# Kernel tuning notes

Measured on AMD Instinct MI355X. Metric: run time of the kernel, lower is better.

Reference implementation:

```python
import jax, jax.numpy as jnp
from jax import lax
import numpy as np

B, NUM_TPM, NUM_CNV, NODE_DIM, DRUG_FEAT = 32, 16000, 16000, 36, 75
N_DRUGS, N_ATOMS, N_PAIRS = 128, 64, 4096


def setup_inputs() -> dict:
    key = jax.random.key(0)
    ks = jax.random.split(key, 32)

    def w(k, shape):
        fan_in = shape[0] if len(shape) == 2 else int(np.prod(shape[1:]))
        return (jax.random.normal(k, shape, jnp.float32) / np.float32(np.sqrt(fan_in))).astype(jnp.float32)

    pic_dim = jax.random.normal(ks[0], (B, 3, 256, 256), jnp.float32)
    rna_seq = jax.random.normal(ks[1], (B, NUM_TPM), jnp.float32)
    gene_cnv = jax.random.normal(ks[2], (B, NUM_CNV), jnp.float32)
    drug_fea = jax.random.uniform(ks[3], (N_DRUGS, N_ATOMS, DRUG_FEAT), jnp.float32)
    a = (jax.random.uniform(ks[4], (N_DRUGS, N_ATOMS, N_ATOMS)) < 0.15).astype(jnp.float32)
    drug_adj = jnp.maximum(a, jnp.transpose(a, (0, 2, 1)))
    index_list = jnp.stack([
        jax.random.randint(ks[5], (N_PAIRS,), 0, B),
        jax.random.randint(ks[6], (N_PAIRS,), 0, N_DRUGS)], axis=1)
    target = jax.random.randint(ks[7], (N_PAIRS,), 0, 2)
    logit_scale = jnp.asarray(10.0, jnp.float32)
    return dict(
        pic_dim=pic_dim, rna_seq=rna_seq, gene_cnv=gene_cnv,
        drug_fea=drug_fea, drug_adj=drug_adj, index_list=index_list,
        target=target, logit_scale=logit_scale,
        conv_w=w(ks[8], (32, 3, 5, 5)), conv_b=jnp.zeros((32,), jnp.float32),
        fc1_w=w(ks[9], (32 * 128 * 128, 1024)), fc1_b=jnp.zeros((1024,), jnp.float32),
        fc2_w=w(ks[10], (1024, 36)), fc2_b=jnp.zeros((36,), jnp.float32),
        mlp1_w1=w(ks[11], (NUM_TPM, NUM_TPM // 4)), mlp1_b1=jnp.zeros((NUM_TPM // 4,), jnp.float32),
        mlp1_w2=w(ks[12], (NUM_TPM // 4, NODE_DIM)), mlp1_b2=jnp.zeros((NODE_DIM,), jnp.float32),
        mlp2_w1=w(ks[13], (NUM_CNV, NUM_CNV // 4)), mlp2_b1=jnp.zeros((NUM_CNV // 4,), jnp.float32),
        mlp2_w2=w(ks[14], (NUM_CNV // 4, NODE_DIM)), mlp2_b2=jnp.zeros((NODE_DIM,), jnp.float32),
        att_w1=w(ks[15], (36, 128)), att_b1=jnp.zeros((128,), jnp.float32),
        att_w2=w(ks[16], (128, 1)),
        end_w1=w(ks[17], (NODE_DIM * 4, NODE_DIM)), end_b1=jnp.zeros((NODE_DIM,), jnp.float32),
        end_w2=w(ks[18], (NODE_DIM, 2)), end_b2=jnp.zeros((2,), jnp.float32),
        gcn_w=w(ks[19], (DRUG_FEAT, NODE_DIM * 8)), gcn_w2=w(ks[20], (NODE_DIM * 8, NODE_DIM * 2)))


def _mlp(x, w1, b1, w2, b2):  # Linear-ReLU-(Dropout eval)-Linear-Softmax
    h = jax.nn.relu(x @ w1 + b1)
    return jax.nn.softmax(h @ w2 + b2, axis=-1)


def _ce(logits, labels):  # mean cross entropy, labels int [N]
    lp = jax.nn.log_softmax(logits, axis=-1)
    return -jnp.take_along_axis(lp, labels[:, None], axis=1).mean()


def reference(pic_dim, rna_seq, gene_cnv, drug_fea, drug_adj, index_list, target,
              logit_scale, conv_w, conv_b, fc1_w, fc1_b, fc2_w, fc2_b,
              mlp1_w1, mlp1_b1, mlp1_w2, mlp1_b2, mlp2_w1, mlp2_b1, mlp2_w2, mlp2_b2,
              att_w1, att_b1, att_w2, end_w1, end_b1, end_w2, end_b2, gcn_w, gcn_w2):
    # omics branches
    rna1 = _mlp(rna_seq, mlp1_w1, mlp1_b1, mlp1_w2, mlp1_b2)    # [B,36]
    cnv1 = _mlp(gene_cnv, mlp2_w1, mlp2_b1, mlp2_w2, mlp2_b2)   # [B,36]
    # image branch: conv(3->32,k5,p2) + relu + maxpool2 + fc
    x = lax.conv_general_dilated(pic_dim, conv_w, (1, 1), [(2, 2), (2, 2)])
    x = jax.nn.relu(x + conv_b[None, :, None, None])
    x = lax.reduce_window(x, -jnp.inf, lax.max, (1, 1, 2, 2), (1, 1, 2, 2), 'VALID')
    x = x.reshape(x.shape[0], -1)                               # [B, 32*128*128]
    x = jax.nn.relu(x @ fc1_w + fc1_b)
    pic1 = x @ fc2_w + fc2_b                                    # [B,36]
    # semantic attention over the two omics views
    z = jnp.stack([rna1, cnv1], axis=1)                         # [B,2,36]
    wv = (jnp.tanh(z @ att_w1 + att_b1) @ att_w2).mean(0)       # [2,1]
    beta = jax.nn.softmax(wv, axis=0)
    cell = (beta[None] * z).sum(1)                              # [B,36]
    # CLIP-style loss
    pic1 = pic1 / jnp.linalg.norm(pic1, axis=1, keepdims=True)
    cell = cell / jnp.linalg.norm(cell, axis=1, keepdims=True)
    image_fea = logit_scale * (pic1 @ cell.T)
    labels = jnp.arange(image_fea.shape[0])
    total_loss2 = (_ce(image_fea, labels) + _ce(image_fea.T, labels)) / 2
    cell_cat = jnp.concatenate([cell, pic1], axis=1)            # [B,72]
    # batched drug GCN (replaces per-drug python loop)
    eye = jnp.eye(N_ATOMS, dtype=jnp.float32)
    def gcn_one(X, A):
        Ht = A.T * (1.0 - eye) + eye        # set diagonal to 1 (add self loops)
        deg = Ht.sum(1)
        dinv = jnp.where(deg == 0, 0.0, 1.0 / deg)
        Hn = dinv[:, None] * Ht             # D^-1 A_hat  (== H.t() after norm)
        out = Hn @ ((Hn @ (X @ gcn_w)) @ gcn_w2)
        return jnp.max(jax.nn.relu(out), axis=0)  # max over atoms -> [72]
    drugfea = jax.vmap(gcn_one)(drug_fea, drug_adj)             # [n_drugs,72]
    # pair prediction head
    Bc = jnp.concatenate([cell_cat[index_list[:, 0]], drugfea[index_list[:, 1]]], axis=1)
    Bp = _mlp(Bc, end_w1, end_b1, end_w2, end_b2)               # [n_pairs,2]
    loss1 = _ce(Bp, target)
    return (loss1, total_loss2, Bp, target)
```

## Files before the change

### kernel.cpp

```cpp
#include <hip/hip_runtime.h>
#include <hip/hip_bf16.h>
#include <math.h>

typedef float evf4 __attribute__((ext_vector_type(4)));
typedef float evf2 __attribute__((ext_vector_type(2)));

__device__ __forceinline__ void fma4(float4& a, float s, const float4& v) {
  a.x += s * v.x; a.y += s * v.y; a.z += s * v.z; a.w += s * v.w;
}
__device__ __forceinline__ float4 ntload4(const float4* p) {
  evf4 v = __builtin_nontemporal_load((const evf4*)p);
  return make_float4(v.x, v.y, v.z, v.w);
}
__device__ __forceinline__ float2 ntload2(const float2* p) {
  evf2 v = __builtin_nontemporal_load((const evf2*)p);
  return make_float2(v.x, v.y);
}

__device__ __forceinline__ void conv_body(
    const float* __restrict__ pic, const float* __restrict__ cw,
    const float* __restrict__ cb, float* __restrict__ pooled,
    int bid, float tile[3][8][260]) {
  int php = bid & 63, ocg2 = (bid >> 6) & 1, b = bid >> 7;
  int tid = threadIdx.x;
  int pw = tid & 127, phl = tid >> 7;
  int ph = php * 2 + phl;
  int h_base = php * 4 - 2;
  for (int i = tid; i < 3 * 8 * 260; i += 256) {
    int c = i % 260; int rr = (i / 260) & 7; int ic = i / (260 * 8);
    int h = h_base + rr, w = c - 2;
    float v = 0.f;
    if (h >= 0 && h < 256 && w >= 0 && w < 256)
      v = pic[((size_t)b * 3 + ic) * 65536 + h * 256 + w];
    tile[ic][rr][c] = v;
  }
  __syncthreads();
  float acc[16][4];
#pragma unroll
  for (int o = 0; o < 16; ++o)
#pragma unroll
    for (int q = 0; q < 4; ++q) acc[o][q] = 0.f;
  int r0 = phl * 2;
  int c0 = pw * 2;
#pragma unroll
  for (int ic = 0; ic < 3; ++ic) {
    float win[6][6];
#pragma unroll
    for (int r = 0; r < 6; ++r)
#pragma unroll
      for (int cc = 0; cc < 6; ++cc) win[r][cc] = tile[ic][r0 + r][c0 + cc];
#pragma unroll
    for (int o = 0; o < 16; ++o) {
      const float* __restrict__ wk = cw + ((ocg2 * 16 + o) * 3 + ic) * 25;
#pragma unroll
      for (int kh = 0; kh < 5; ++kh)
#pragma unroll
        for (int kw = 0; kw < 5; ++kw) {
          float wv = wk[kh * 5 + kw];
          acc[o][0] += win[kh][kw] * wv;
          acc[o][1] += win[kh][kw + 1] * wv;
          acc[o][2] += win[kh + 1][kw] * wv;
          acc[o][3] += win[kh + 1][kw + 1] * wv;
        }
    }
  }
#pragma unroll
  for (int o = 0; o < 16; ++o) {
    float m = fmaxf(fmaxf(acc[o][0], acc[o][1]), fmaxf(acc[o][2], acc[o][3]));
    m = fmaxf(m + cb[ocg2 * 16 + o], 0.f);
    pooled[(((size_t)b * 32 + ocg2 * 16 + o) * 128 + ph) * 128 + pw] = m;
  }
}

__device__ __forceinline__ void wc_body(
    const float* __restrict__ w1, const float* __restrict__ w2,
    float* __restrict__ wc, int bx) {
  int i = bx * 256 + threadIdx.x;
  if (i >= 75 * 72) return;
  int r = i / 72, c = i - r * 72;
  float s = 0.f;
  for (int k = 0; k < 288; ++k) s += w1[r * 288 + k] * w2[k * 72 + c];
  wc[i] = s;
}

__global__ __launch_bounds__(256) void k1_conv_wc_kernel(
    const float* __restrict__ pic, const float* __restrict__ cw,
    const float* __restrict__ cb, float* __restrict__ pooled,
    const float* __restrict__ gw, const float* __restrict__ gw2,
    float* __restrict__ wcb) {
  __shared__ float tile[3][8][260];
  int bid = blockIdx.x;
  if (bid < 4096) conv_body(pic, cw, cb, pooled, bid, tile);
  else            wc_body(gw, gw2, wcb, bid - 4096);
}

__device__ __forceinline__ void gemm2c_body(
    const float* __restrict__ X, const float* __restrict__ W,
    float* __restrict__ partial, int K, int N, int chunk,
    int bx, int split, float xs[128][36]) {
  int tid = threadIdx.x;
  int colv = bx * 256 + tid;
  int col0 = colv * 2;
  bool active = col0 < N;
  int k0 = split * chunk, k1 = min(k0 + chunk, K);
  size_t Nv = (size_t)(N >> 1);
  const float2* Wv = (const float2*)W;
  float2 acc[32];
#pragma unroll
  for (int b = 0; b < 32; ++b) acc[b] = make_float2(0.f, 0.f);

  auto fmablk = [&](int kk, const float2& w2) {
    const float4* xr = (const float4*)xs[kk];
#pragma unroll
    for (int b4 = 0; b4 < 8; ++b4) {
      float4 xv = xr[b4];
      acc[b4 * 4 + 0].x += xv.x * w2.x; acc[b4 * 4 + 0].y += xv.x * w2.y;
      acc[b4 * 4 + 1].x += xv.y * w2.x; acc[b4 * 4 + 1].y += xv.y * w2.y;
      acc[b4 * 4 + 2].x += xv.z * w2.x; acc[b4 * 4 + 2].y += xv.z * w2.y;
      acc[b4 * 4 + 3].x += xv.w * w2.x; acc[b4 * 4 + 3].y += xv.w * w2.y;
    }
  };

  for (int kt = k0; kt < k1; kt += 128) {
    __syncthreads();
#pragma unroll
    for (int j = 0; j < 4; ++j) {
      int idx = tid + j * 256;
      int b = idx >> 5, kk = (idx & 31) * 4;
      float4 x = *(const float4*)&X[(size_t)b * K + kt + kk];
      xs[kk + 0][b] = x.x; xs[kk + 1][b] = x.y;
      xs[kk + 2][b] = x.z; xs[kk + 3][b] = x.w;
    }
    __syncthreads();
    if (active) {
      const float2* wp = Wv + (size_t)kt * Nv + colv;
      float2 cur[8], nxt[8];
#pragma unroll
      for (int j = 0; j < 8; ++j) cur[j] = ntload2(wp + (size_t)j * Nv);
#pragma unroll 1
      for (int g = 0; g < 15; ++g) {
        const float2* wn = wp + 8 * Nv;
#pragma unroll
        for (int j = 0; j < 8; ++j) nxt[j] = ntload2(wn + (size_t)j * Nv);
        int kb = g * 8;
#pragma unroll
        for (int j = 0; j < 8; ++j) fmablk(kb + j, cur[j]);
#pragma unroll
        for (int j = 0; j < 8; ++j) cur[j] = nxt[j];
        wp = wn;
      }
#pragma unroll
      for (int j = 0; j < 8; ++j) fmablk(120 + j, cur[j]);
    }
  }
  if (active) {
    float* p = partial + (size_t)split * 32 * N + col0;
#pragma unroll
    for (int b = 0; b < 32; ++b) *(float2*)(p + (size_t)b * N) = acc[b];
  }
}

__global__ __launch_bounds__(256) void gemm_all_kernel(
    const float* __restrict__ pooled, const float* __restrict__ fc1w,
    float* __restrict__ pfc1,
    const float* __restrict__ rna, const float* __restrict__ m1w1, float* __restrict__ pm1,
    const float* __restrict__ cnv, const float* __restrict__ m2w1, float* __restrict__ pm2) {
  __shared__ float xs[128][36];
  int b = blockIdx.x;
  if (b < 512) {
    gemm2c_body(pooled, fc1w, pfc1, 524288, 1024, 2048, b & 1, b >> 1, xs);
  } else {
    int j = b - 512;
    int z = j / 504;
    int r = j % 504;
    int bx = r & 7, split = r >> 3;
    if (z == 0) gemm2c_body(rna, m1w1, pm1, 16000, 4000, 256, bx, split, xs);
    else        gemm2c_body(cnv, m2w1, pm2, 16000, 4000, 256, bx, split, xs);
  }
}

__device__ __forceinline__ void fadd4(float4& a, const float4& v) {
  a.x += v.x; a.y += v.y; a.z += v.z; a.w += v.w;
}

__device__ __forceinline__ void reduce_s1_body(
    const float* __restrict__ partial, float* __restrict__ p2,
    int bx, int sy) {
  int i = bx * 256 + threadIdx.x;
  const float4* p = (const float4*)partial + (size_t)(sy * 128) * 8192 + i;
  const size_t st = 8192;
  float4 s0 = make_float4(0, 0, 0, 0), s1 = s0, s2 = s0, s3 = s0;
  for (int sp = 0; sp < 128; sp += 4) {
    fadd4(s0, ntload4(p + (sp + 0) * st));
    fadd4(s1, ntload4(p + (sp + 1) * st));
    fadd4(s2, ntload4(p + (sp + 2) * st));
    fadd4(s3, ntload4(p + (sp + 3) * st));
  }
  float4 r;
  r.x = (s0.x + s1.x) + (s2.x + s3.x);
  r.y = (s0.y + s1.y) + (s2.y + s3.y);
  r.z = (s0.z + s1.z) + (s2.z + s3.z);
  r.w = (s0.w + s1.w) + (s2.w + s3.w);
  ((float4*)p2)[(size_t)sy * 8192 + i] = r;
}

__device__ __forceinline__ void reduce_mlp_body(
    const float* __restrict__ partial, const float* __restrict__ bias,
    float* __restrict__ out, int bx) {
  int i = bx * 256 + threadIdx.x;
  if (i >= 32000) return;
  const float4* p = (const float4*)partial + i;
  const size_t st = 32000;
  float4 s0 = make_float4(0, 0, 0, 0), s1 = s0, s2 = s0, s3 = s0;
  int sp = 0;
  for (; sp + 4 <= 63; sp += 4) {
    fadd4(s0, ntload4(p + (sp + 0) * st));
    fadd4(s1, ntload4(p + (sp + 1) * st));
    fadd4(s2, ntload4(p + (sp + 2) * st));
    fadd4(s3, ntload4(p + (sp + 3) * st));
  }
  for (; sp < 63; ++sp) fadd4(s0, ntload4(p + (size_t)sp * st));
  float4 bi = ((const float4*)bias)[i % 1000];
  float4 r;
  r.x = fmaxf(bi.x + (s0.x + s1.x) + (s2.x + s3.x), 0.f);
  r.y = fmaxf(bi.y + (s0.y + s1.y) + (s2.y + s3.y), 0.f);
  r.z = fmaxf(bi.z + (s0.z + s1.z) + (s2.z + s3.z), 0.f);
  r.w = fmaxf(bi.w + (s0.w + s1.w) + (s2.w + s3.w), 0.f);
  ((float4*)out)[i] = r;
}

__global__ __launch_bounds__(256) void k3_reduce_kernel(
    const float* __restrict__ pfc1, float* __restrict__ p2fc1,
    const float* __restrict__ pm1, const float* __restrict__ m1b1, float* __restrict__ h1,
    const float* __restrict__ pm2, const float* __restrict__ m2b1, float* __restrict__ h2) {
  int b = blockIdx.x;
  if (b < 64) {
    reduce_s1_body(pfc1, p2fc1, b & 31, b >> 5);
  } else {
    int idx = b - 64;
    if (idx < 125) reduce_mlp_body(pm1, m1b1, h1, idx);
    else           reduce_mlp_body(pm2, m2b1, h2, idx - 125);
  }
}

__device__ __forceinline__ void reduce_s2_body(
    const float* __restrict__ p2, const float* __restrict__ bias,
    float* __restrict__ out, int bx) {
  int i = bx * 256 + threadIdx.x;
  float4 a = ((const float4*)p2)[i];
  float4 b = ((const float4*)p2)[8192 + i];
  float4 bi = ((const float4*)bias)[i & 255];
  float4 r;
  r.x = fmaxf(bi.x + a.x + b.x, 0.f);
  r.y = fmaxf(bi.y + a.y + b.y, 0.f);
  r.z = fmaxf(bi.z + a.z + b.z, 0.f);
  r.w = fmaxf(bi.w + a.w + b.w, 0.f);
  ((float4*)out)[i] = r;
}

__device__ __forceinline__ void gcn_body(
    const float* __restrict__ Xg, const float* __restrict__ Ag,
    const float* __restrict__ Wc, float* __restrict__ drugfea, int d,
    float Hn[64][65], float Xs[64][75], float Wcs[75][72],
    float Ys[64][72], float Ts[64][72]) {
  int tid = threadIdx.x;
  const float* Ad = Ag + (size_t)d * 4096;
  const float* Xd = Xg + (size_t)d * 4800;
  for (int i = tid; i < 4096; i += 256) {
    int r = i & 63, c = i >> 6;
    Hn[r][c] = (r == c) ? 1.f : Ad[c * 64 + r];
  }
  for (int i = tid; i < 4800; i += 256) Xs[i / 75][i % 75] = Xd[i];
  for (int i = tid; i < 5400; i += 256) Wcs[i / 72][i % 72] = Wc[i];
  __syncthreads();
  if (tid < 64) {
    float s = 0.f;
    for (int c = 0; c < 64; ++c) s += Hn[tid][c];
    float inv = (s == 0.f) ? 0.f : 1.f / s;
    for (int c = 0; c < 64; ++c) Hn[tid][c] *= inv;
  }
  __syncthreads();
  int rb = tid >> 3, cb = tid & 7;
  int r0 = rb * 2, c0 = cb * 9;
  {
    float o0[9], o1[9];
#pragma unroll
    for (int j = 0; j < 9; ++j) { o0[j] = 0.f; o1[j] = 0.f; }
    for (int k = 0; k < 75; ++k) {
      float x0 = Xs[r0][k], x1 = Xs[r0 + 1][k];
#pragma unroll
      for (int j = 0; j < 9; ++j) {
        float w = Wcs[k][c0 + j];
        o0[j] += x0 * w; o1[j] += x1 * w;
      }
    }
#pragma unroll
    for (int j = 0; j < 9; ++j) { Ys[r0][c0 + j] = o0[j]; Ys[r0 + 1][c0 + j] = o1[j]; }
  }
  __syncthreads();
  {
    float o0[9], o1[9];
#pragma unroll
    for (int j = 0; j < 9; ++j) { o0[j] = 0.f; o1[j] = 0.f; }
    for (int k = 0; k < 64; ++k) {
      float x0 = Hn[r0][k], x1 = Hn[r0 + 1][k];
#pragma unroll
      for (int j = 0; j < 9; ++j) {
        float w = Ys[k][c0 + j];
        o0[j] += x0 * w; o1[j] += x1 * w;
      }
    }
#pragma unroll
    for (int j = 0; j < 9; ++j) { Ts[r0][c0 + j] = o0[j]; Ts[r0 + 1][c0 + j] = o1[j]; }
  }
  __syncthreads();
  {
    float o0[9], o1[9];
#pragma unroll
    for (int j = 0; j < 9; ++j) { o0[j] = 0.f; o1[j] = 0.f; }
    for (int k = 0; k < 64; ++k) {
      float x0 = Hn[r0][k], x1 = Hn[r0 + 1][k];
#pragma unroll
      for (int j = 0; j < 9; ++j) {
        float w = Ts[k][c0 + j];
        o0[j] += x0 * w; o1[j] += x1 * w;
      }
    }
#pragma unroll
    for (int j = 0; j < 9; ++j) {
      Ys[r0][c0 + j] = fmaxf(o0[j], 0.f);
      Ys[r0 + 1][c0 + j] = fmaxf(o1[j], 0.f);
    }
  }
  __syncthreads();
  if (tid < 72) {
    float m = Ys[0][tid];
    for (int i = 1; i < 64; ++i) m = fmaxf(m, Ys[i][tid]);
    drugfea[d * 72 + tid] = m;
  }
}

__global__ __launch_bounds__(256) void k4_s2_gcn_kernel(
    const float* __restrict__ p2fc1, const float* __restrict__ fc1_b,
    float* __restrict__ fcact,
    const float* __restrict__ Xg, const float* __restrict__ Ag,
    const float* __restrict__ wcb, float* __restrict__ drugfea) {
  __shared__ float Hn[64][65];
  __shared__ float Xs[64][75];
  __shared__ float Wcs[75][72];
  __shared__ float Ys[64][72];
  __shared__ float Ts[64][72];
  int b = blockIdx.x;
  if (b < 32) reduce_s2_body(p2fc1, fc1_b, fcact, b);
  else        gcn_body(Xg, Ag, wcb, drugfea, b - 32, Hn, Xs, Wcs, Ys, Ts);
}

__global__ __launch_bounds__(256) void lin36_all_kernel(
    const float* __restrict__ X0, const float* __restrict__ W0,
    const float* __restrict__ bi0, float* __restrict__ out0,
    const float* __restrict__ X1, const float* __restrict__ W1,
    const float* __restrict__ bi1, float* __restrict__ out1,
    const float* __restrict__ X2, const float* __restrict__ W2,
    const float* __restrict__ bi2, float* __restrict__ out2) {
  const float* X; const float* W; const float* bias; float* out; int K; bool do_sm;
  if (blockIdx.y == 0)      { X = X0; W = W0; bias = bi0; out = out0; K = 4000; do_sm = true; }
  else if (blockIdx.y == 1) { X = X1; W = W1; bias = bi1; out = out1; K = 4000; do_sm = true; }
  else                      { X = X2; W = W2; bias = bi2; out = out2; K = 1024; do_sm = false; }
  __shared__ float xs[4000];
  __shared__ float red[28][36];
  __shared__ float vals[36];
  __shared__ float mxv, smv;
  int b = blockIdx.x, tid = threadIdx.x;
  for (int i = tid; i < K; i += 256) xs[i] = X[(size_t)b * K + i];
  __syncthreads();
  if (tid < 252) {
    int c4 = tid % 9, g = tid / 9;
    const float4* W4 = (const float4*)W;
    float4 s = make_float4(0.f, 0.f, 0.f, 0.f);
    for (int k = g; k < K; k += 28) fma4(s, xs[k], W4[k * 9 + c4]);
    red[g][c4 * 4 + 0] = s.x; red[g][c4 * 4 + 1] = s.y;
    red[g][c4 * 4 + 2] = s.z; red[g][c4 * 4 + 3] = s.w;
  }
  __syncthreads();
  if (tid < 36) {
    float s = bias[tid];
    for (int g = 0; g < 28; ++g) s += red[g][tid];
    vals[tid] = s;
  }
  __syncthreads();
  if (do_sm) {
    if (tid == 0) {
      float m = -1e30f;
      for (int j = 0; j < 36; ++j) m = fmaxf(m, vals[j]);
      float e = 0.f;
      for (int j = 0; j < 36; ++j) e += expf(vals[j] - m);
      mxv = m; smv = e;
    }
    __syncthreads();
    if (tid < 36) out[b * 36 + tid] = expf(vals[tid] - mxv) / smv;
  } else {
    if (tid < 36) out[b * 36 + tid] = vals[tid];
  }
}

__global__ __launch_bounds__(256) void head_kernel(
    const float* __restrict__ rna1, const float* __restrict__ cnv1,
    const float* __restrict__ pic1r, const float* __restrict__ aw1,
    const float* __restrict__ ab1, const float* __restrict__ aw2,
    const float* __restrict__ scale_p, float* __restrict__ cell_cat,
    float* __restrict__ dout) {
  __shared__ float z[2][32][36];
  __shared__ float pic1n[32][36];
  __shared__ float celln[32][36];
  __shared__ float fea[32][32];
  __shared__ float wvp[64];
  __shared__ float beta0, beta1;
  __shared__ float rowl[32], coll[32];
  int tid = threadIdx.x;
  for (int i = tid; i < 1152; i += 256) {
    int b = i / 36, k = i - (i / 36) * 36;
    z[0][b][k] = rna1[i];
    z[1][b][k] = cnv1[i];
    pic1n[b][k] = pic1r[i];
  }
  __syncthreads();
  {
    int p = tid >> 2, sub = tid & 3;
    int b = p >> 1, v = p & 1;
    float s = 0.f;
    for (int h = sub; h < 128; h += 4) {
      float a = ab1[h];
      for (int k = 0; k < 36; ++k) a += z[v][b][k] * aw1[k * 128 + h];
      s += tanhf(a) * aw2[h];
    }
    s += __shfl_down(s, 1, 64);
    s += __shfl_down(s, 2, 64);
    if (sub == 0) wvp[p] = s;
  }
  __syncthreads();
  if (tid == 0) {
    float w0 = 0.f, w1 = 0.f;
    for (int b = 0; b < 32; ++b) { w0 += wvp[b * 2]; w1 += wvp[b * 2 + 1]; }
    w0 /= 32.f; w1 /= 32.f;
    float m = fmaxf(w0, w1);
    float e0 = expf(w0 - m), e1 = expf(w1 - m);
    beta0 = e0 / (e0 + e1); beta1 = e1 / (e0 + e1);
  }
  __syncthreads();
  for (int i = tid; i < 1152; i += 256) {
    int b = i / 36, k = i - (i / 36) * 36;
    celln[b][k] = beta0 * z[0][b][k] + beta1 * z[1][b][k];
  }
  __syncthreads();
  if (tid < 32) {
    float s = 0.f;
    for (int k = 0; k < 36; ++k) { float x = pic1n[tid][k]; s += x * x; }
    float inv = 1.f / sqrtf(s);
    for (int k = 0; k < 36; ++k) pic1n[tid][k] *= inv;
  } else if (tid < 64) {
    int b = tid - 32;
    float s = 0.f;
    for (int k = 0; k < 36; ++k) { float x = celln[b][k]; s += x * x; }
    float inv = 1.f / sqrtf(s);
    for (int k = 0; k < 36; ++k) celln[b][k] *= inv;
  }
  __syncthreads();
  for (int i = tid; i < 1152; i += 256) {
    int b = i / 36, k = i - (i / 36) * 36;
    cell_cat[b * 72 + k] = celln[b][k];
    cell_cat[b * 72 + 36 + k] = pic1n[b][k];
  }
  float sc = *scale_p;
  for (int t = tid; t < 1024; t += 256) {
    int i = t >> 5, j = t & 31;
    float s = 0.f;
    for (int k = 0; k < 36; ++k) s += pic1n[i][k] * celln[j][k];
    fea[i][j] = sc * s;
  }
  __syncthreads();
  if (tid < 32) {
    float m = -1e30f;
    for (int j = 0; j < 32; ++j) m = fmaxf(m, fea[tid][j]);
    float e = 0.f;
    for (int j = 0; j < 32; ++j) e += expf(fea[tid][j] - m);
    rowl[tid] = (logf(e) + m) - fea[tid][tid];
  } else if (tid < 64) {
    int j = tid - 32;
    float m = -1e30f;
    for (int i = 0; i < 32; ++i) m = fmaxf(m, fea[i][j]);
    float e = 0.f;
    for (int i = 0; i < 32; ++i) e += expf(fea[i][j] - m);
    coll[j] = (logf(e) + m) - fea[j][j];
  }
  __syncthreads();
  if (tid == 0) {
    float s1 = 0.f, s2 = 0.f;
    for (int i = 0; i < 32; ++i) { s1 += rowl[i]; s2 += coll[i]; }
    dout[1] = 0.5f * (s1 / 32.f + s2 / 32.f);
  }
}

__global__ __launch_bounds__(256) void pair_kernel(
    const float* __restrict__ cell_cat, const float* __restrict__ drugfea,
    const int* __restrict__ idx, const int* __restrict__ target,
    const float* __restrict__ w1, const float* __restrict__ b1,
    const float* __restrict__ w2, const float* __restrict__ b2,
    float* __restrict__ bp_out, float* __restrict__ tgt_out,
    float* __restrict__ blocksums) {
  __shared__ float w1s[144][36];
  __shared__ float ccs[32][73];
  __shared__ float dfs[128][73];
  __shared__ float w2s[72], b2s[2];
  __shared__ float lsum[256];
  int tid = threadIdx.x;
  {
    float4* dst = (float4*)&w1s[0][0];
    const float4* src = (const float4*)w1;
    for (int i = tid; i < 1296; i += 256) dst[i] = src[i];
  }
  for (int i = tid; i < 2304; i += 256) ccs[i / 72][i % 72] = cell_cat[i];
  for (int i = tid; i < 9216; i += 256) dfs[i / 72][i % 72] = drugfea[i];
  if (tid < 72) w2s[tid] = w2[tid];
  if (tid < 2) b2s[tid] = b2[tid];
  __syncthreads();
  int p = blockIdx.x * 256 + tid;
  int ci = idx[p * 2], dj = idx[p * 2 + 1];
  float4 h4[9];
  {
    const float4* bb = (const float4*)b1;
#pragma unroll
    for (int q = 0; q < 9; ++q) h4[q] = bb[q];
  }
  for (int k = 0; k < 72; ++k) {
    float x = ccs[ci][k];
    const float4* wr = (const float4*)&w1s[k][0];
#pragma unroll
    for (int q = 0; q < 9; ++q) fma4(h4[q], x, wr[q]);
  }
  for (int k = 0; k < 72; ++k) {
    float x = dfs[dj][k];
    const float4* wr = (const float4*)&w1s[72 + k][0];
#pragma unroll
    for (int q = 0; q < 9; ++q) fma4(h4[q], x, wr[q]);
  }
  float l0 = b2s[0], l1 = b2s[1];
#pragma unroll
  for (int q = 0; q < 9; ++q) {
    float hv;
    hv = fmaxf(h4[q].x, 0.f); l0 += hv * w2s[(q * 4 + 0) * 2]; l1 += hv * w2s[(q * 4 + 0) * 2 + 1];
    hv = fmaxf(h4[q].y, 0.f); l0 += hv * w2s[(q * 4 + 1) * 2]; l1 += hv * w2s[(q * 4 + 1) * 2 + 1];
    hv = fmaxf(h4[q].z, 0.f); l0 += hv * w2s[(q * 4 + 2) * 2]; l1 += hv * w2s[(q * 4 + 2) * 2 + 1];
    hv = fmaxf(h4[q].w, 0.f); l0 += hv * w2s[(q * 4 + 3) * 2]; l1 += hv * w2s[(q * 4 + 3) * 2 + 1];
  }
  float m = fmaxf(l0, l1);
  float e0 = expf(l0 - m), e1 = expf(l1 - m);
  float inv = 1.f / (e0 + e1);
  float p0 = e0 * inv, p1 = e1 * inv;
  bp_out[p * 2] = p0;
  bp_out[p * 2 + 1] = p1;
  int t = target[p];
  float mm = fmaxf(p0, p1);
  float lse = logf(expf(p0 - mm) + expf(p1 - mm)) + mm;
  float chosen = t ? p1 : p0;
  lsum[tid] = lse - chosen;
  tgt_out[p] = (float)t;
  __syncthreads();
  for (int s = 128; s > 0; s >>= 1) {
    if (tid < s) lsum[tid] += lsum[tid + s];
    __syncthreads();
  }
  if (tid == 0) blocksums[blockIdx.x] = lsum[0];
}

__global__ void final_kernel(const float* __restrict__ blocksums, float* __restrict__ dout) {
  if (threadIdx.x == 0 && blockIdx.x == 0) {
    float s = 0.f;
    for (int i = 0; i < 16; ++i) s += blocksums[i];
    dout[0] = s / 4096.f;
  }
}

extern "C" void kernel_launch(void* const* d_in, const int* in_sizes, int n_in,
                              void* d_out, int out_size, void* d_ws, size_t ws_size,
                              hipStream_t stream) {
  (void)in_sizes; (void)n_in; (void)out_size; (void)ws_size;
  const float* pic        = (const float*)d_in[0];
  const float* rna        = (const float*)d_in[1];
  const float* cnv        = (const float*)d_in[2];
  const float* drug_fea   = (const float*)d_in[3];
  const float* drug_adj   = (const float*)d_in[4];
  const int*   index_list = (const int*)d_in[5];
  const int*   target     = (const int*)d_in[6];
  const float* logit_scale= (const float*)d_in[7];
  const float* conv_w     = (const float*)d_in[8];
  const float* conv_b     = (const float*)d_in[9];
  const float* fc1_w      = (const float*)d_in[10];
  const float* fc1_b      = (const float*)d_in[11];
  const float* fc2_w      = (const float*)d_in[12];
  const float* fc2_b      = (const float*)d_in[13];
  const float* m1w1       = (const float*)d_in[14];
  const float* m1b1       = (const float*)d_in[15];
  const float* m1w2       = (const float*)d_in[16];
  const float* m1b2       = (const float*)d_in[17];
  const float* m2w1       = (const float*)d_in[18];
  const float* m2b1       = (const float*)d_in[19];
  const float* m2w2       = (const float*)d_in[20];
  const float* m2b2       = (const float*)d_in[21];
  const float* aw1        = (const float*)d_in[22];
  const float* ab1        = (const float*)d_in[23];
  const float* aw2        = (const float*)d_in[24];
  const float* ew1        = (const float*)d_in[25];
  const float* eb1        = (const float*)d_in[26];
  const float* ew2        = (const float*)d_in[27];
  const float* eb2        = (const float*)d_in[28];
  const float* gw         = (const float*)d_in[29];
  const float* gw2        = (const float*)d_in[30];

  float* ws = (float*)d_ws;
  float* pooled  = ws;
  float* pfc1    = ws + 16777216;
  float* p2fc1   = ws + 33554432;
  float* pm1     = ws + 33685504;
  float* pm2     = ws + 41749504;
  float* fcact   = ws + 49813504;
  float* h1      = ws + 49846272;
  float* h2      = ws + 49974272;
  float* rna1    = ws + 50102272;
  float* cnv1    = ws + 50103424;
  float* pic1r   = ws + 50104576;
  float* wcb     = ws + 50105728;
  float* drugf   = ws + 50111128;
  float* cellcat = ws + 50120344;
  float* bsums   = ws + 50122648;

  float* out = (float*)d_out;

  k1_conv_wc_kernel<<<4118, 256, 0, stream>>>(pic, conv_w, conv_b, pooled,
                                              gw, gw2, wcb);
  gemm_all_kernel<<<1520, 256, 0, stream>>>(pooled, fc1_w, pfc1,
                                            rna, m1w1, pm1, cnv, m2w1, pm2);
  k3_reduce_kernel<<<314, 256, 0, stream>>>(pfc1, p2fc1,
                                            pm1, m1b1, h1, pm2, m2b1, h2);
  k4_s2_gcn_kernel<<<160, 256, 0, stream>>>(p2fc1, fc1_b, fcact,
                                            drug_fea, drug_adj, wcb, drugf);
  {
    dim3 g(32, 3);
    lin36_all_kernel<<<g, 256, 0, stream>>>(h1, m1w2, m1b2, rna1,
                                            h2, m2w2, m2b2, cnv1,
                                            fcact, fc2_w, fc2_b, pic1r);
  }
  head_kernel<<<1, 256, 0, stream>>>(rna1, cnv1, pic1r, aw1, ab1, aw2,
                                     logit_scale, cellcat, out);
  pair_kernel<<<16, 256, 0, stream>>>(cellcat, drugf, index_list, target,
                                      ew1, eb1, ew2, eb2,
                                      out + 2, out + 2 + 8192, bsums);
  final_kernel<<<1, 64, 0, stream>>>(bsums, out);
}
```

Measured before the change: 1.122 ms.

## Widen GEMM tiles to four columns per thread and prefetch activation tiles

The split-K GEMM body now computes four output columns per thread with float4 weight loads instead of two with float2. This halves the number of column blocks and doubles the number of K-splits for fc1, which becomes 512 splits of 1024 each, so the reduction kernels gain blocks and sum four partial sets. The next activation tile is prefetched into registers during compute so global latency is hidden behind the weight stream. The cost is higher register pressure (128 accumulator floats per thread), which may lower occupancy.

```diff
diff --git a/kernel.cpp b/kernel.cpp
--- a/kernel.cpp
+++ b/kernel.cpp
@@ -3,18 +3,16 @@
 #include <math.h>
 
 typedef float evf4 __attribute__((ext_vector_type(4)));
-typedef float evf2 __attribute__((ext_vector_type(2)));
 
 __device__ __forceinline__ void fma4(float4& a, float s, const float4& v) {
   a.x += s * v.x; a.y += s * v.y; a.z += s * v.z; a.w += s * v.w;
+}
+__device__ __forceinline__ void fadd4(float4& a, const float4& v) {
+  a.x += v.x; a.y += v.y; a.z += v.z; a.w += v.w;
 }
 __device__ __forceinline__ float4 ntload4(const float4* p) {
   evf4 v = __builtin_nontemporal_load((const evf4*)p);
   return make_float4(v.x, v.y, v.z, v.w);
-}
-__device__ __forceinline__ float2 ntload2(const float2* p) {
-  evf2 v = __builtin_nontemporal_load((const evf2*)p);
-  return make_float2(v.x, v.y);
 }
 
 __device__ __forceinline__ void conv_body(
@@ -94,30 +92,38 @@
   else            wc_body(gw, gw2, wcb, bid - 4096);
 }
 
-__device__ __forceinline__ void gemm2c_body(
+__device__ __forceinline__ void gemm32p_body(
     const float* __restrict__ X, const float* __restrict__ W,
     float* __restrict__ partial, int K, int N, int chunk,
     int bx, int split, float xs[128][36]) {
   int tid = threadIdx.x;
   int colv = bx * 256 + tid;
-  int col0 = colv * 2;
+  int col0 = colv * 4;
   bool active = col0 < N;
   int k0 = split * chunk, k1 = min(k0 + chunk, K);
-  size_t Nv = (size_t)(N >> 1);
-  const float2* Wv = (const float2*)W;
-  float2 acc[32];
-#pragma unroll
-  for (int b = 0; b < 32; ++b) acc[b] = make_float2(0.f, 0.f);
-
-  auto fmablk = [&](int kk, const float2& w2) {
+  size_t Nv = (size_t)(N >> 2);
+  const float4* Wv = (const float4*)W;
+  float4 acc[32];
+#pragma unroll
+  for (int b = 0; b < 32; ++b) acc[b] = make_float4(0.f, 0.f, 0.f, 0.f);
+
+  float4 xpre[4];
+#pragma unroll
+  for (int j = 0; j < 4; ++j) {
+    int idx = tid + j * 256;
+    int b = idx >> 5, kk = (idx & 31) * 4;
+    xpre[j] = *(const float4*)&X[(size_t)b * K + k0 + kk];
+  }
+
+  auto fmablk = [&](int kk, const float4& w4) {
     const float4* xr = (const float4*)xs[kk];
 #pragma unroll
     for (int b4 = 0; b4 < 8; ++b4) {
       float4 xv = xr[b4];
-      acc[b4 * 4 + 0].x += xv.x * w2.x; acc[b4 * 4 + 0].y += xv.x * w2.y;
-      acc[b4 * 4 + 1].x += xv.y * w2.x; acc[b4 * 4 + 1].y += xv.y * w2.y;
-      acc[b4 * 4 + 2].x += xv.z * w2.x; acc[b4 * 4 + 2].y += xv.z * w2.y;
-      acc[b4 * 4 + 3].x += xv.w * w2.x; acc[b4 * 4 + 3].y += xv.w * w2.y;
+      fma4(acc[b4 * 4 + 0], xv.x, w4);
+      fma4(acc[b4 * 4 + 1], xv.y, w4);
+      fma4(acc[b4 * 4 + 2], xv.z, w4);
+      fma4(acc[b4 * 4 + 3], xv.w, w4);
     }
   };
 
@@ -127,21 +133,30 @@
     for (int j = 0; j < 4; ++j) {
       int idx = tid + j * 256;
       int b = idx >> 5, kk = (idx & 31) * 4;
-      float4 x = *(const float4*)&X[(size_t)b * K + kt + kk];
-      xs[kk + 0][b] = x.x; xs[kk + 1][b] = x.y;
-      xs[kk + 2][b] = x.z; xs[kk + 3][b] = x.w;
+      xs[kk + 0][b] = xpre[j].x;
+      xs[kk + 1][b] = xpre[j].y;
+      xs[kk + 2][b] = xpre[j].z;
+      xs[kk + 3][b] = xpre[j].w;
     }
     __syncthreads();
+    if (kt + 128 < k1) {
+#pragma unroll
+      for (int j = 0; j < 4; ++j) {
+        int idx = tid + j * 256;
+        int b = idx >> 5, kk = (idx & 31) * 4;
+        xpre[j] = *(const float4*)&X[(size_t)b * K + kt + 128 + kk];
+      }
+    }
     if (active) {
-      const float2* wp = Wv + (size_t)kt * Nv + colv;
-      float2 cur[8], nxt[8];
-#pragma unroll
-      for (int j = 0; j < 8; ++j) cur[j] = ntload2(wp + (size_t)j * Nv);
+      const float4* wp = Wv + (size_t)kt * Nv + colv;
+      float4 cur[8], nxt[8];
+#pragma unroll
+      for (int j = 0; j < 8; ++j) cur[j] = ntload4(wp + (size_t)j * Nv);
 #pragma unroll 1
       for (int g = 0; g < 15; ++g) {
-        const float2* wn = wp + 8 * Nv;
-#pragma unroll
-        for (int j = 0; j < 8; ++j) nxt[j] = ntload2(wn + (size_t)j * Nv);
+        const float4* wn = wp + 8 * Nv;
+#pragma unroll
+        for (int j = 0; j < 8; ++j) nxt[j] = ntload4(wn + (size_t)j * Nv);
         int kb = g * 8;
 #pragma unroll
         for (int j = 0; j < 8; ++j) fmablk(kb + j, cur[j]);
@@ -156,7 +171,7 @@
   if (active) {
     float* p = partial + (size_t)split * 32 * N + col0;
 #pragma unroll
-    for (int b = 0; b < 32; ++b) *(float2*)(p + (size_t)b * N) = acc[b];
+    for (int b = 0; b < 32; ++b) *(float4*)(p + (size_t)b * N) = acc[b];
   }
 }
 
@@ -168,19 +183,15 @@
   __shared__ float xs[128][36];
   int b = blockIdx.x;
   if (b < 512) {
-    gemm2c_body(pooled, fc1w, pfc1, 524288, 1024, 2048, b & 1, b >> 1, xs);
+    gemm32p_body(pooled, fc1w, pfc1, 524288, 1024, 1024, 0, b, xs);
   } else {
     int j = b - 512;
-    int z = j / 504;
-    int r = j % 504;
-    int bx = r & 7, split = r >> 3;
-    if (z == 0) gemm2c_body(rna, m1w1, pm1, 16000, 4000, 256, bx, split, xs);
-    else        gemm2c_body(cnv, m2w1, pm2, 16000, 4000, 256, bx, split, xs);
-  }
-}
-
-__device__ __forceinline__ void fadd4(float4& a, const float4& v) {
-  a.x += v.x; a.y += v.y; a.z += v.z; a.w += v.w;
+    int z = j / 252;
+    int r = j % 252;
+    int bx = r & 3, split = r >> 2;
+    if (z == 0) gemm32p_body(rna, m1w1, pm1, 16000, 4000, 256, bx, split, xs);
+    else        gemm32p_body(cnv, m2w1, pm2, 16000, 4000, 256, bx, split, xs);
+  }
 }
 
 __device__ __forceinline__ void reduce_s1_body(
@@ -234,10 +245,10 @@
     const float* __restrict__ pm1, const float* __restrict__ m1b1, float* __restrict__ h1,
     const float* __restrict__ pm2, const float* __restrict__ m2b1, float* __restrict__ h2) {
   int b = blockIdx.x;
-  if (b < 64) {
+  if (b < 128) {
     reduce_s1_body(pfc1, p2fc1, b & 31, b >> 5);
   } else {
-    int idx = b - 64;
+    int idx = b - 128;
     if (idx < 125) reduce_mlp_body(pm1, m1b1, h1, idx);
     else           reduce_mlp_body(pm2, m2b1, h2, idx - 125);
   }
@@ -249,12 +260,14 @@
   int i = bx * 256 + threadIdx.x;
   float4 a = ((const float4*)p2)[i];
   float4 b = ((const float4*)p2)[8192 + i];
+  float4 c = ((const float4*)p2)[16384 + i];
+  float4 d = ((const float4*)p2)[24576 + i];
   float4 bi = ((const float4*)bias)[i & 255];
   float4 r;
-  r.x = fmaxf(bi.x + a.x + b.x, 0.f);
-  r.y = fmaxf(bi.y + a.y + b.y, 0.f);
-  r.z = fmaxf(bi.z + a.z + b.z, 0.f);
-  r.w = fmaxf(bi.w + a.w + b.w, 0.f);
+  r.x = fmaxf(bi.x + (a.x + b.x) + (c.x + d.x), 0.f);
+  r.y = fmaxf(bi.y + (a.y + b.y) + (c.y + d.y), 0.f);
+  r.z = fmaxf(bi.z + (a.z + b.z) + (c.z + d.z), 0.f);
+  r.w = fmaxf(bi.w + (a.w + b.w) + (c.w + d.w), 0.f);
   ((float4*)out)[i] = r;
 }
 
@@ -637,9 +650,9 @@
 
   k1_conv_wc_kernel<<<4118, 256, 0, stream>>>(pic, conv_w, conv_b, pooled,
                                               gw, gw2, wcb);
-  gemm_all_kernel<<<1520, 256, 0, stream>>>(pooled, fc1_w, pfc1,
+  gemm_all_kernel<<<1016, 256, 0, stream>>>(pooled, fc1_w, pfc1,
                                             rna, m1w1, pm1, cnv, m2w1, pm2);
-  k3_reduce_kernel<<<314, 256, 0, stream>>>(pfc1, p2fc1,
+  k3_reduce_kernel<<<378, 256, 0, stream>>>(pfc1, p2fc1,
                                             pm1, m1b1, h1, pm2, m2b1, h2);
   k4_s2_gcn_kernel<<<160, 256, 0, stream>>>(p2fc1, fc1_b, fcact,
                                             drug_fea, drug_adj, wcb, drugf);
```

Measured after the change: 1.007 ms, median of 2. -10.3%, faster.
